# Kernel optimization log

Hardware: AMD Instinct MI355X
Metric: run time of the kernel (lower is better)

## Reference

```python
import jax, jax.numpy as jnp
import numpy as np

B, IN_E, IN_I, D = 4096, 4096, 4096, 2048
IN_BR = 8192
BS = IN_BR // D  # block size = 4
K_E, K_I = 50, 1
E_TO_I = 50.0
BN_EPS = 1e-5


def setup_inputs() -> dict:
    key = jax.random.key(0)
    ks = jax.random.split(key, 8)
    # fan-in uniform init like nn.Linear (kaiming-uniform bound ~ 1/sqrt(in))
    def linw(k, out_f, in_f):
        b = 1.0 / np.sqrt(in_f)
        return jax.random.uniform(k, (out_f, in_f), jnp.float32, -b, b)
    return {
        "excitatory_input": jax.random.normal(ks[0], (B, IN_E), jnp.float32),
        "inhibitory_input": jax.random.normal(ks[1], (B, IN_I), jnp.float32),
        "dendrite_branch_outputs": jax.random.uniform(ks[2], (B, IN_BR), jnp.float32),
        "w_exc": linw(ks[3], D, IN_E),
        "w_inh": linw(ks[4], D, IN_I),
        "w_block": linw(ks[5], D, IN_BR),
        "bn_gamma": jnp.ones((D,), jnp.float32),
        "bn_beta": jnp.zeros((D,), jnp.float32),
    }


def _topk_linear(x, w, k):
    # keep the k largest weights per output row, zero the rest, then matmul
    idx = jax.lax.top_k(w, k)[1]                          # [D, k]
    mask = jnp.zeros_like(w).at[jnp.arange(w.shape[0])[:, None], idx].set(1.0)
    return x @ (w * mask).T                               # [B, D]


def _block_linear(x, w):
    # block-diagonal mask: row c uses columns [c*BS, (c+1)*BS)
    out_f = w.shape[0]
    wb = w.reshape(out_f, out_f, BS)[jnp.arange(out_f), jnp.arange(out_f)]  # [D, BS]
    xb = x.reshape(x.shape[0], out_f, BS)                                   # [B, D, BS]
    return jnp.einsum('bds,ds->bd', xb, wb)


def reference(excitatory_input, inhibitory_input, dendrite_branch_outputs,
              w_exc, w_inh, w_block, bn_gamma, bn_beta):
    dendrite_excitation = _topk_linear(excitatory_input, w_exc, K_E)
    dendrite_inhibition = _topk_linear(inhibitory_input, w_inh, K_I)
    dendrite_depolarization = _block_linear(dendrite_branch_outputs, w_block)
    total_excitatory = dendrite_excitation + dendrite_depolarization
    # neuron_type == 'excitatory'
    act = total_excitatory - E_TO_I * dendrite_inhibition
    # BatchNorm1d, training mode: batch stats, biased variance
    mean = jnp.mean(act, axis=0)
    var = jnp.var(act, axis=0)
    act = (act - mean) * jax.lax.rsqrt(var + BN_EPS) * bn_gamma + bn_beta
    return jax.nn.sigmoid(act)
```

## Files before the change

kernel.cpp:

```cpp
#include <hip/hip_runtime.h>
#include <hip/hip_fp16.h>

#define B_     4096
#define INE_   4096
#define INBR_  8192
#define D_     2048
#define KE_    50
#define KPAD_  52
#define CAP_   512

__device__ __forceinline__ unsigned packh2(float a, float b) {
  __half2 h = __floats2half2_rn(a, b);
  return __builtin_bit_cast(unsigned, h);
}
__device__ __forceinline__ float2 unpackh2(unsigned u) {
  __half2 h = __builtin_bit_cast(__half2, u);
  return __half22float2(h);
}

__device__ void topk_body(const float* __restrict__ W, int row, int k, int kpad,
                          float hi, float t0, float vscale,
                          unsigned* __restrict__ out_off, float* __restrict__ out_val)
{
  const int t = threadIdx.x;
  const float* wr = W + (size_t)row * INE_;

  __shared__ float cval[CAP_];
  __shared__ int   ccol[CAP_];
  __shared__ int   scnt;
  __shared__ int   red[4];

  float thr = t0;
  int M = 0;
  for (int attempt = 0; attempt < 8; ++attempt) {
    int local = 0;
    #pragma unroll
    for (int j = 0; j < 4; ++j) {
      float4 w4 = *reinterpret_cast<const float4*>(wr + 4 * (t + 256 * j));
      local += (w4.x > thr) + (w4.y > thr) + (w4.z > thr) + (w4.w > thr);
    }
    #pragma unroll
    for (int off = 32; off > 0; off >>= 1) local += __shfl_down(local, off);
    if ((t & 63) == 0) red[t >> 6] = local;
    __syncthreads();
    M = red[0] + red[1] + red[2] + red[3];
    __syncthreads();
    if (M >= k && M <= CAP_) break;
    if (M < k) thr = hi - (hi - thr) * 4.0f;
    else       thr = hi - (hi - thr) * 0.5f;
  }

  if (t == 0) scnt = 0;
  __syncthreads();
  #pragma unroll
  for (int j = 0; j < 4; ++j) {
    int cbase = 4 * (t + 256 * j);
    float4 w4 = *reinterpret_cast<const float4*>(wr + cbase);
    float wv[4] = {w4.x, w4.y, w4.z, w4.w};
    #pragma unroll
    for (int q = 0; q < 4; ++q) {
      if (wv[q] > thr) {
        int pp = atomicAdd(&scnt, 1);
        if (pp < CAP_) { cval[pp] = wv[q]; ccol[pp] = cbase + q; }
      }
    }
  }
  __syncthreads();
  M = scnt < CAP_ ? scnt : CAP_;

  for (int i = t; i < M; i += 256) {
    float wi = cval[i]; int ci = ccol[i];
    int rank = 0;
    for (int m = 0; m < M; ++m) {
      float wm = cval[m]; int cm = ccol[m];
      rank += (wm > wi || (wm == wi && cm < ci)) ? 1 : 0;
    }
    if (rank < k) {
      unsigned c = (unsigned)ci;
      unsigned off = ((c >> 2) << 4) | ((c & 3u) << 14);
      float    val = wi * vscale;
      if (kpad == 1) {
        out_off[row] = off;
        out_val[row] = val;
      } else {
        size_t idx = ((size_t)(rank >> 2) * D_ + row) * 4 + (rank & 3);
        out_off[idx] = off;
        out_val[idx] = val;
      }
    }
  }
  if (kpad > 1 && t < kpad - k) {
    int slot = k + t;
    size_t idx = ((size_t)(slot >> 2) * D_ + row) * 4 + (slot & 3);
    out_off[idx] = 0u;
    out_val[idx] = 0.0f;
  }
}

__global__ __launch_bounds__(256) void prep_kernel(
    const float* __restrict__ wexc, const float* __restrict__ winh,
    const float* __restrict__ wblk,
    unsigned* __restrict__ soT, float* __restrict__ veT,
    unsigned* __restrict__ so_inh, float* __restrict__ vi_inh,
    float* __restrict__ wdiag)
{
  const int bid = blockIdx.x;
  const float hi = 0.015625f;
  if (bid < 2048) {
    topk_body(wexc, bid, KE_, KPAD_, hi, hi * (1.0f - 200.0f / 4096.0f), 1.0f,
              soT, veT);
  } else if (bid < 4096) {
    topk_body(winh, bid - 2048, 1, 1, hi, hi * (1.0f - 48.0f / 4096.0f), -50.0f,
              so_inh, vi_inh);
  } else {
    const int t = threadIdx.x;
    #pragma unroll
    for (int j = 0; j < 8; ++j) {
      int d = t + 256 * j;
      float4 w = *reinterpret_cast<const float4*>(wblk + (size_t)d * (INBR_ + 4));
      reinterpret_cast<float4*>(wdiag)[d] = w;
    }
  }
}

__device__ __forceinline__ void stage_rows8(const float* __restrict__ src,
                                            unsigned* xs, int b0, int p, int Q) {
  const float* r0p = src + (size_t)(b0 + 2 * p)     * INE_;
  const float* r1p = src + (size_t)(b0 + 2 * p + 1) * INE_;
  #pragma unroll
  for (int m = 0; m < 8; ++m) {
    int c0 = 4 * Q + 512 * m;
    float4 fa = *reinterpret_cast<const float4*>(r0p + c0);
    float4 fb = *reinterpret_cast<const float4*>(r1p + c0);
    int wb = 4 * (Q + 128 * m) + p;
    xs[wb]          = packh2(fa.x, fb.x);
    xs[wb + 4096]   = packh2(fa.y, fb.y);
    xs[wb + 8192]   = packh2(fa.z, fb.z);
    xs[wb + 12288]  = packh2(fa.w, fb.w);
  }
}

__device__ __forceinline__ uint4 ld16(const char* ldsb, unsigned off) {
  return *reinterpret_cast<const uint4*>(ldsb + off);
}

#define FMA8(R, G, WV) do {                                                \
    float2 f0 = unpackh2((G).x), f1 = unpackh2((G).y);                     \
    float2 f2 = unpackh2((G).z), f3 = unpackh2((G).w);                     \
    acc[R][0] = fmaf(f0.x, (WV), acc[R][0]);                               \
    acc[R][1] = fmaf(f0.y, (WV), acc[R][1]);                               \
    acc[R][2] = fmaf(f1.x, (WV), acc[R][2]);                               \
    acc[R][3] = fmaf(f1.y, (WV), acc[R][3]);                               \
    acc[R][4] = fmaf(f2.x, (WV), acc[R][4]);                               \
    acc[R][5] = fmaf(f2.y, (WV), acc[R][5]);                               \
    acc[R][6] = fmaf(f3.x, (WV), acc[R][6]);                               \
    acc[R][7] = fmaf(f3.y, (WV), acc[R][7]);                               \
  } while (0)

__global__ __launch_bounds__(512, 4) void ei_kernel(
    const float* __restrict__ xe, const float* __restrict__ xi,
    const unsigned* __restrict__ soT, const float* __restrict__ veT,
    const unsigned* __restrict__ so_inh, const float* __restrict__ vi_inh,
    float* __restrict__ act)
{
  __shared__ unsigned xs[16384];
  const int t  = threadIdx.x;
  const int b0 = blockIdx.x * 8;
  const int p  = t & 3;
  const int Q  = t >> 2;

  float acc[4][8];
  #pragma unroll
  for (int r = 0; r < 4; ++r)
    #pragma unroll
    for (int b = 0; b < 8; ++b) acc[r][b] = 0.0f;

  const char* ldsb = reinterpret_cast<const char*>(xs);
  const uint4*  soT4 = reinterpret_cast<const uint4*>(soT);
  const float4* veT4 = reinterpret_cast<const float4*>(veT);

  stage_rows8(xe, xs, b0, p, Q);
  __syncthreads();
  for (int ii = 0; ii < KPAD_ / 4; ++ii) {
    uint4 o[4]; float4 v[4];
    #pragma unroll
    for (int r = 0; r < 4; ++r) {
      o[r] = soT4[ii * D_ + t + 512 * r];
      v[r] = veT4[ii * D_ + t + 512 * r];
    }
    {
      uint4 g[2][4];
      #pragma unroll
      for (int rr = 0; rr < 2; ++rr) {
        g[rr][0] = ld16(ldsb, o[rr].x);
        g[rr][1] = ld16(ldsb, o[rr].y);
        g[rr][2] = ld16(ldsb, o[rr].z);
        g[rr][3] = ld16(ldsb, o[rr].w);
      }
      #pragma unroll
      for (int rr = 0; rr < 2; ++rr) {
        FMA8(rr, g[rr][0], v[rr].x);
        FMA8(rr, g[rr][1], v[rr].y);
        FMA8(rr, g[rr][2], v[rr].z);
        FMA8(rr, g[rr][3], v[rr].w);
      }
    }
    {
      uint4 g[2][4];
      #pragma unroll
      for (int rr = 0; rr < 2; ++rr) {
        g[rr][0] = ld16(ldsb, o[2 + rr].x);
        g[rr][1] = ld16(ldsb, o[2 + rr].y);
        g[rr][2] = ld16(ldsb, o[2 + rr].z);
        g[rr][3] = ld16(ldsb, o[2 + rr].w);
      }
      #pragma unroll
      for (int rr = 0; rr < 2; ++rr) {
        FMA8(2 + rr, g[rr][0], v[2 + rr].x);
        FMA8(2 + rr, g[rr][1], v[2 + rr].y);
        FMA8(2 + rr, g[rr][2], v[2 + rr].z);
        FMA8(2 + rr, g[rr][3], v[2 + rr].w);
      }
    }
  }
  __syncthreads();

  stage_rows8(xi, xs, b0, p, Q);
  unsigned oi[4]; float viv[4];
  #pragma unroll
  for (int r = 0; r < 4; ++r) {
    oi[r]  = so_inh[t + 512 * r];
    viv[r] = vi_inh[t + 512 * r];
  }
  __syncthreads();
  {
    uint4 gi[4];
    #pragma unroll
    for (int r = 0; r < 4; ++r) gi[r] = ld16(ldsb, oi[r]);
    #pragma unroll
    for (int r = 0; r < 4; ++r) FMA8(r, gi[r], viv[r]);
  }

  #pragma unroll
  for (int r = 0; r < 4; ++r) {
    const int d = t + 512 * r;
    #pragma unroll
    for (int b = 0; b < 8; ++b)
      act[(size_t)(b0 + b) * D_ + d] = acc[r][b];
  }
}

__global__ __launch_bounds__(256) void br_kernel(
    const float* __restrict__ xbr, const float* __restrict__ wdiag,
    float* __restrict__ act)
{
  const float4* xbr4 = reinterpret_cast<const float4*>(xbr);
  const float4* wd4  = reinterpret_cast<const float4*>(wdiag);
  float4*       act4 = reinterpret_cast<float4*>(act);
  const int total = B_ * D_ / 4;
  for (int i = blockIdx.x * 256 + threadIdx.x; i < total;
       i += gridDim.x * 256) {
    int b  = i >> 9;
    int dq = i & 511;
    float4 a = act4[i];
    const float4* xp = xbr4 + (size_t)b * (INBR_ / 4) + 4 * dq;
    float4 x0 = xp[0], x1 = xp[1], x2 = xp[2], x3 = xp[3];
    float4 w0 = wd4[4 * dq], w1 = wd4[4 * dq + 1],
           w2 = wd4[4 * dq + 2], w3 = wd4[4 * dq + 3];
    a.x += x0.x * w0.x + x0.y * w0.y + x0.z * w0.z + x0.w * w0.w;
    a.y += x1.x * w1.x + x1.y * w1.y + x1.z * w1.z + x1.w * w1.w;
    a.z += x2.x * w2.x + x2.y * w2.y + x2.z * w2.z + x2.w * w2.w;
    a.w += x3.x * w3.x + x3.y * w3.y + x3.z * w3.z + x3.w * w3.w;
    act4[i] = a;
  }
}

__global__ __launch_bounds__(256) void reduce_stats(
    const float* __restrict__ act, float* __restrict__ sums,
    float* __restrict__ sumsq)
{
  const int dg = blockIdx.x & 63;
  const int rg = blockIdx.x >> 6;
  const int tx = threadIdx.x & 31;
  const int ty = threadIdx.x >> 5;
  const int d  = dg * 32 + tx;

  float s = 0.0f, s2 = 0.0f;
  #pragma unroll 4
  for (int i = 0; i < 64; ++i) {
    int row = rg * 512 + ty + 8 * i;
    float a = act[(size_t)row * D_ + d];
    s += a;
    s2 = fmaf(a, a, s2);
  }
  __shared__ float ls[2][8][32];
  ls[0][ty][tx] = s;
  ls[1][ty][tx] = s2;
  __syncthreads();
  if (ty == 0) {
    #pragma unroll
    for (int j = 1; j < 8; ++j) { s += ls[0][j][tx]; s2 += ls[1][j][tx]; }
    atomicAdd(&sums[d], s);
    atomicAdd(&sumsq[d], s2);
  }
}

__global__ __launch_bounds__(256) void tail_kernel(
    float* __restrict__ act, const float* __restrict__ sums,
    const float* __restrict__ sumsq, const float* __restrict__ gamma,
    const float* __restrict__ beta)
{
  __shared__ float scsh[2 * D_];
  const int tid = threadIdx.x;
  #pragma unroll
  for (int j = 0; j < 8; ++j) {
    int d = tid + 256 * j;
    float mean = sums[d]  * (1.0f / B_);
    float var  = sumsq[d] * (1.0f / B_) - mean * mean;
    float rstd = rsqrtf(var + 1e-5f);
    float sc   = gamma[d] * rstd;
    scsh[2 * d]     = sc;
    scsh[2 * d + 1] = fmaf(-mean, sc, beta[d]);
  }
  __syncthreads();

  const int r0 = blockIdx.x * 8;
  for (int rr = 0; rr < 8; ++rr) {
    float4* rowp = reinterpret_cast<float4*>(act + (size_t)(r0 + rr) * D_);
    #pragma unroll
    for (int i2 = 0; i2 < 2; ++i2) {
      int i = tid + 256 * i2;
      float4 a = rowp[i];
      const float4* sp = reinterpret_cast<const float4*>(scsh + 8 * i);
      float4 s0 = sp[0];
      float4 s1 = sp[1];
      float z0 = fmaf(a.x, s0.x, s0.y);
      float z1 = fmaf(a.y, s0.z, s0.w);
      float z2 = fmaf(a.z, s1.x, s1.y);
      float z3 = fmaf(a.w, s1.z, s1.w);
      a.x = 1.0f / (1.0f + __expf(-z0));
      a.y = 1.0f / (1.0f + __expf(-z1));
      a.z = 1.0f / (1.0f + __expf(-z2));
      a.w = 1.0f / (1.0f + __expf(-z3));
      rowp[i] = a;
    }
  }
}

extern "C" void kernel_launch(void* const* d_in, const int* in_sizes, int n_in,
                              void* d_out, int out_size, void* d_ws, size_t ws_size,
                              hipStream_t stream) {
  const float* xe    = (const float*)d_in[0];
  const float* xi    = (const float*)d_in[1];
  const float* xbr   = (const float*)d_in[2];
  const float* wexc  = (const float*)d_in[3];
  const float* winh  = (const float*)d_in[4];
  const float* wblk  = (const float*)d_in[5];
  const float* gamma = (const float*)d_in[6];
  const float* beta  = (const float*)d_in[7];
  float* act = (float*)d_out;

  char* ws = (char*)d_ws;
  unsigned* soT    = (unsigned*)(ws + 0);
  float*    veT    = (float*)   (ws + 425984);
  unsigned* so_inh = (unsigned*)(ws + 851968);
  float*    vi_inh = (float*)   (ws + 860160);
  float*    wdiag  = (float*)   (ws + 868352);
  float*    sums   = (float*)   (ws + 901120);
  float*    sumsq  = (float*)   (ws + 909312);

  hipMemsetAsync(sums, 0, 2 * D_ * sizeof(float), stream);

  prep_kernel<<<dim3(4097), dim3(256), 0, stream>>>(
      wexc, winh, wblk, soT, veT, so_inh, vi_inh, wdiag);
  ei_kernel<<<dim3(B_ / 8), dim3(512), 0, stream>>>(
      xe, xi, soT, veT, so_inh, vi_inh, act);
  br_kernel<<<dim3(2048), dim3(256), 0, stream>>>(xbr, wdiag, act);
  reduce_stats<<<dim3(512), dim3(256), 0, stream>>>(act, sums, sumsq);
  tail_kernel<<<dim3(512), dim3(256), 0, stream>>>(
      act, sums, sumsq, gamma, beta);
}
```

Measured before the change: 135.7 us.

## Fuse branch term into EI kernel, pack top-k metadata into fp16 records

Result: faster. 131.7 us (-2.9%).

```diff
diff --git a/kernel.cpp b/kernel.cpp
--- a/kernel.cpp
+++ b/kernel.cpp
@@ -20,6 +20,7 @@
 
 __device__ void topk_body(const float* __restrict__ W, int row, int k, int kpad,
                           float hi, float t0, float vscale,
+                          uint4* __restrict__ muT,
                           unsigned* __restrict__ out_off, float* __restrict__ out_val)
 {
   const int t = threadIdx.x;
@@ -78,29 +79,29 @@
     if (rank < k) {
       unsigned c = (unsigned)ci;
       unsigned off = ((c >> 2) << 4) | ((c & 3u) << 14);
-      float    val = wi * vscale;
       if (kpad == 1) {
         out_off[row] = off;
-        out_val[row] = val;
+        out_val[row] = wi * vscale;
       } else {
-        size_t idx = ((size_t)(rank >> 2) * D_ + row) * 4 + (rank & 3);
-        out_off[idx] = off;
-        out_val[idx] = val;
+        char* rec = (char*)muT + ((size_t)(rank >> 2) * D_ + row) * 16;
+        reinterpret_cast<unsigned short*>(rec)[rank & 3] = (unsigned short)off;
+        reinterpret_cast<__half*>(rec)[4 + (rank & 3)] =
+            __float2half_rn(wi * vscale);
       }
     }
   }
   if (kpad > 1 && t < kpad - k) {
     int slot = k + t;
-    size_t idx = ((size_t)(slot >> 2) * D_ + row) * 4 + (slot & 3);
-    out_off[idx] = 0u;
-    out_val[idx] = 0.0f;
+    char* rec = (char*)muT + ((size_t)(slot >> 2) * D_ + row) * 16;
+    reinterpret_cast<unsigned short*>(rec)[slot & 3] = 0;
+    reinterpret_cast<__half*>(rec)[4 + (slot & 3)] = __float2half_rn(0.0f);
   }
 }
 
 __global__ __launch_bounds__(256) void prep_kernel(
     const float* __restrict__ wexc, const float* __restrict__ winh,
     const float* __restrict__ wblk,
-    unsigned* __restrict__ soT, float* __restrict__ veT,
+    uint4* __restrict__ muT,
     unsigned* __restrict__ so_inh, float* __restrict__ vi_inh,
     float* __restrict__ wdiag)
 {
@@ -108,10 +109,10 @@
   const float hi = 0.015625f;
   if (bid < 2048) {
     topk_body(wexc, bid, KE_, KPAD_, hi, hi * (1.0f - 200.0f / 4096.0f), 1.0f,
-              soT, veT);
+              muT, nullptr, nullptr);
   } else if (bid < 4096) {
     topk_body(winh, bid - 2048, 1, 1, hi, hi * (1.0f - 48.0f / 4096.0f), -50.0f,
-              so_inh, vi_inh);
+              nullptr, so_inh, vi_inh);
   } else {
     const int t = threadIdx.x;
     #pragma unroll
@@ -157,9 +158,10 @@
     acc[R][7] = fmaf(f3.y, (WV), acc[R][7]);                               \
   } while (0)
 
-__global__ __launch_bounds__(512, 4) void ei_kernel(
+__global__ __launch_bounds__(512, 4) void fused_ei(
     const float* __restrict__ xe, const float* __restrict__ xi,
-    const unsigned* __restrict__ soT, const float* __restrict__ veT,
+    const float* __restrict__ xbr, const float* __restrict__ wdiag,
+    const uint4* __restrict__ muT,
     const unsigned* __restrict__ so_inh, const float* __restrict__ vi_inh,
     float* __restrict__ act)
 {
@@ -176,63 +178,97 @@
     for (int b = 0; b < 8; ++b) acc[r][b] = 0.0f;
 
   const char* ldsb = reinterpret_cast<const char*>(xs);
-  const uint4*  soT4 = reinterpret_cast<const uint4*>(soT);
-  const float4* veT4 = reinterpret_cast<const float4*>(veT);
 
   stage_rows8(xe, xs, b0, p, Q);
-  __syncthreads();
+
+  float4 xia[4], xib[4];
+  {
+    const float* xr0 = xi + (size_t)(b0 + 2 * p)     * INE_;
+    const float* xr1 = xi + (size_t)(b0 + 2 * p + 1) * INE_;
+    #pragma unroll
+    for (int m = 0; m < 4; ++m) {
+      xia[m] = *reinterpret_cast<const float4*>(xr0 + 4 * Q + 512 * m);
+      xib[m] = *reinterpret_cast<const float4*>(xr1 + 4 * Q + 512 * m);
+    }
+  }
+  unsigned oi[4]; float viv[4];
+  #pragma unroll
+  for (int r = 0; r < 4; ++r) {
+    oi[r]  = so_inh[t + 512 * r];
+    viv[r] = vi_inh[t + 512 * r];
+  }
+  __syncthreads();
+
   for (int ii = 0; ii < KPAD_ / 4; ++ii) {
-    uint4 o[4]; float4 v[4];
-    #pragma unroll
-    for (int r = 0; r < 4; ++r) {
-      o[r] = soT4[ii * D_ + t + 512 * r];
-      v[r] = veT4[ii * D_ + t + 512 * r];
-    }
+    uint4 m[4];
+    #pragma unroll
+    for (int r = 0; r < 4; ++r) m[r] = muT[ii * D_ + t + 512 * r];
     {
       uint4 g[2][4];
       #pragma unroll
       for (int rr = 0; rr < 2; ++rr) {
-        g[rr][0] = ld16(ldsb, o[rr].x);
-        g[rr][1] = ld16(ldsb, o[rr].y);
-        g[rr][2] = ld16(ldsb, o[rr].z);
-        g[rr][3] = ld16(ldsb, o[rr].w);
+        g[rr][0] = ld16(ldsb, m[rr].x & 0xFFFFu);
+        g[rr][1] = ld16(ldsb, m[rr].x >> 16);
+        g[rr][2] = ld16(ldsb, m[rr].y & 0xFFFFu);
+        g[rr][3] = ld16(ldsb, m[rr].y >> 16);
       }
       #pragma unroll
       for (int rr = 0; rr < 2; ++rr) {
-        FMA8(rr, g[rr][0], v[rr].x);
-        FMA8(rr, g[rr][1], v[rr].y);
-        FMA8(rr, g[rr][2], v[rr].z);
-        FMA8(rr, g[rr][3], v[rr].w);
+        float2 vA = unpackh2(m[rr].z);
+        float2 vB = unpackh2(m[rr].w);
+        FMA8(rr, g[rr][0], vA.x);
+        FMA8(rr, g[rr][1], vA.y);
+        FMA8(rr, g[rr][2], vB.x);
+        FMA8(rr, g[rr][3], vB.y);
       }
     }
     {
       uint4 g[2][4];
       #pragma unroll
       for (int rr = 0; rr < 2; ++rr) {
-        g[rr][0] = ld16(ldsb, o[2 + rr].x);
-        g[rr][1] = ld16(ldsb, o[2 + rr].y);
-        g[rr][2] = ld16(ldsb, o[2 + rr].z);
-        g[rr][3] = ld16(ldsb, o[2 + rr].w);
+        g[rr][0] = ld16(ldsb, m[2 + rr].x & 0xFFFFu);
+        g[rr][1] = ld16(ldsb, m[2 + rr].x >> 16);
+        g[rr][2] = ld16(ldsb, m[2 + rr].y & 0xFFFFu);
+        g[rr][3] = ld16(ldsb, m[2 + rr].y >> 16);
       }
       #pragma unroll
       for (int rr = 0; rr < 2; ++rr) {
-        FMA8(2 + rr, g[rr][0], v[2 + rr].x);
-        FMA8(2 + rr, g[rr][1], v[2 + rr].y);
-        FMA8(2 + rr, g[rr][2], v[2 + rr].z);
-        FMA8(2 + rr, g[rr][3], v[2 + rr].w);
-      }
-    }
-  }
-  __syncthreads();
-
-  stage_rows8(xi, xs, b0, p, Q);
-  unsigned oi[4]; float viv[4];
-  #pragma unroll
-  for (int r = 0; r < 4; ++r) {
-    oi[r]  = so_inh[t + 512 * r];
-    viv[r] = vi_inh[t + 512 * r];
-  }
-  __syncthreads();
+        float2 vA = unpackh2(m[2 + rr].z);
+        float2 vB = unpackh2(m[2 + rr].w);
+        FMA8(2 + rr, g[rr][0], vA.x);
+        FMA8(2 + rr, g[rr][1], vA.y);
+        FMA8(2 + rr, g[rr][2], vB.x);
+        FMA8(2 + rr, g[rr][3], vB.y);
+      }
+    }
+  }
+  __syncthreads();
+
+  #pragma unroll
+  for (int m = 0; m < 4; ++m) {
+    int wb = 4 * (Q + 128 * m) + p;
+    xs[wb]          = packh2(xia[m].x, xib[m].x);
+    xs[wb + 4096]   = packh2(xia[m].y, xib[m].y);
+    xs[wb + 8192]   = packh2(xia[m].z, xib[m].z);
+    xs[wb + 12288]  = packh2(xia[m].w, xib[m].w);
+  }
+  {
+    const float* xr0 = xi + (size_t)(b0 + 2 * p)     * INE_;
+    const float* xr1 = xi + (size_t)(b0 + 2 * p + 1) * INE_;
+    #pragma unroll
+    for (int m = 4; m < 8; ++m) {
+      int c0 = 4 * Q + 512 * m;
+      float4 fa = *reinterpret_cast<const float4*>(xr0 + c0);
+      float4 fb = *reinterpret_cast<const float4*>(xr1 + c0);
+      int wb = 4 * (Q + 128 * m) + p;
+      xs[wb]          = packh2(fa.x, fb.x);
+      xs[wb + 4096]   = packh2(fa.y, fb.y);
+      xs[wb + 8192]   = packh2(fa.z, fb.z);
+      xs[wb + 12288]  = packh2(fa.w, fb.w);
+    }
+  }
+  __syncthreads();
+
   {
     uint4 gi[4];
     #pragma unroll
@@ -244,34 +280,21 @@
   #pragma unroll
   for (int r = 0; r < 4; ++r) {
     const int d = t + 512 * r;
+    float4 wb4 = reinterpret_cast<const float4*>(wdiag)[d];
+    #pragma unroll
+    for (int b = 0; b < 8; ++b) {
+      float4 xb4 = *reinterpret_cast<const float4*>(
+          xbr + (size_t)(b0 + b) * INBR_ + 4 * d);
+      acc[r][b] += xb4.x * wb4.x + xb4.y * wb4.y + xb4.z * wb4.z + xb4.w * wb4.w;
+    }
+  }
+
+  #pragma unroll
+  for (int r = 0; r < 4; ++r) {
+    const int d = t + 512 * r;
     #pragma unroll
     for (int b = 0; b < 8; ++b)
       act[(size_t)(b0 + b) * D_ + d] = acc[r][b];
-  }
-}
-
-__global__ __launch_bounds__(256) void br_kernel(
-    const float* __restrict__ xbr, const float* __restrict__ wdiag,
-    float* __restrict__ act)
-{
-  const float4* xbr4 = reinterpret_cast<const float4*>(xbr);
-  const float4* wd4  = reinterpret_cast<const float4*>(wdiag);
-  float4*       act4 = reinterpret_cast<float4*>(act);
-  const int total = B_ * D_ / 4;
-  for (int i = blockIdx.x * 256 + threadIdx.x; i < total;
-       i += gridDim.x * 256) {
-    int b  = i >> 9;
-    int dq = i & 511;
-    float4 a = act4[i];
-    const float4* xp = xbr4 + (size_t)b * (INBR_ / 4) + 4 * dq;
-    float4 x0 = xp[0], x1 = xp[1], x2 = xp[2], x3 = xp[3];
-    float4 w0 = wd4[4 * dq], w1 = wd4[4 * dq + 1],
-           w2 = wd4[4 * dq + 2], w3 = wd4[4 * dq + 3];
-    a.x += x0.x * w0.x + x0.y * w0.y + x0.z * w0.z + x0.w * w0.w;
-    a.y += x1.x * w1.x + x1.y * w1.y + x1.z * w1.z + x1.w * w1.w;
-    a.z += x2.x * w2.x + x2.y * w2.y + x2.z * w2.z + x2.w * w2.w;
-    a.w += x3.x * w3.x + x3.y * w3.y + x3.z * w3.z + x3.w * w3.w;
-    act4[i] = a;
   }
 }
 
@@ -306,9 +329,9 @@
 }
 
 __global__ __launch_bounds__(256) void tail_kernel(
-    float* __restrict__ act, const float* __restrict__ sums,
-    const float* __restrict__ sumsq, const float* __restrict__ gamma,
-    const float* __restrict__ beta)
+    const float* __restrict__ act, float* __restrict__ out,
+    const float* __restrict__ sums, const float* __restrict__ sumsq,
+    const float* __restrict__ gamma, const float* __restrict__ beta)
 {
   __shared__ float scsh[2 * D_];
   const int tid = threadIdx.x;
@@ -326,11 +349,12 @@
 
   const int r0 = blockIdx.x * 8;
   for (int rr = 0; rr < 8; ++rr) {
-    float4* rowp = reinterpret_cast<float4*>(act + (size_t)(r0 + rr) * D_);
+    const float4* ap = reinterpret_cast<const float4*>(act + (size_t)(r0 + rr) * D_);
+    float4*       op = reinterpret_cast<float4*>(out + (size_t)(r0 + rr) * D_);
     #pragma unroll
     for (int i2 = 0; i2 < 2; ++i2) {
       int i = tid + 256 * i2;
-      float4 a = rowp[i];
+      float4 a = ap[i];
       const float4* sp = reinterpret_cast<const float4*>(scsh + 8 * i);
       float4 s0 = sp[0];
       float4 s1 = sp[1];
@@ -338,11 +362,12 @@
       float z1 = fmaf(a.y, s0.z, s0.w);
       float z2 = fmaf(a.z, s1.x, s1.y);
       float z3 = fmaf(a.w, s1.z, s1.w);
-      a.x = 1.0f / (1.0f + __expf(-z0));
-      a.y = 1.0f / (1.0f + __expf(-z1));
-      a.z = 1.0f / (1.0f + __expf(-z2));
-      a.w = 1.0f / (1.0f + __expf(-z3));
-      rowp[i] = a;
+      float4 o;
+      o.x = 1.0f / (1.0f + __expf(-z0));
+      o.y = 1.0f / (1.0f + __expf(-z1));
+      o.z = 1.0f / (1.0f + __expf(-z2));
+      o.w = 1.0f / (1.0f + __expf(-z3));
+      op[i] = o;
     }
   }
 }
@@ -358,25 +383,24 @@
   const float* wblk  = (const float*)d_in[5];
   const float* gamma = (const float*)d_in[6];
   const float* beta  = (const float*)d_in[7];
-  float* act = (float*)d_out;
+  float* out = (float*)d_out;
 
   char* ws = (char*)d_ws;
-  unsigned* soT    = (unsigned*)(ws + 0);
-  float*    veT    = (float*)   (ws + 425984);
-  unsigned* so_inh = (unsigned*)(ws + 851968);
-  float*    vi_inh = (float*)   (ws + 860160);
-  float*    wdiag  = (float*)   (ws + 868352);
-  float*    sums   = (float*)   (ws + 901120);
-  float*    sumsq  = (float*)   (ws + 909312);
+  uint4*    muT    = (uint4*)   (ws + 0);
+  unsigned* so_inh = (unsigned*)(ws + 425984);
+  float*    vi_inh = (float*)   (ws + 434176);
+  float*    wdiag  = (float*)   (ws + 442368);
+  float*    sums   = (float*)   (ws + 475136);
+  float*    sumsq  = (float*)   (ws + 483328);
+  float*    act    = (float*)   (ws + 1048576);
 
   hipMemsetAsync(sums, 0, 2 * D_ * sizeof(float), stream);
 
   prep_kernel<<<dim3(4097), dim3(256), 0, stream>>>(
-      wexc, winh, wblk, soT, veT, so_inh, vi_inh, wdiag);
-  ei_kernel<<<dim3(B_ / 8), dim3(512), 0, stream>>>(
-      xe, xi, soT, veT, so_inh, vi_inh, act);
-  br_kernel<<<dim3(2048), dim3(256), 0, stream>>>(xbr, wdiag, act);
+      wexc, winh, wblk, muT, so_inh, vi_inh, wdiag);
+  fused_ei<<<dim3(B_ / 8), dim3(512), 0, stream>>>(
+      xe, xi, xbr, wdiag, muT, so_inh, vi_inh, act);
   reduce_stats<<<dim3(512), dim3(256), 0, stream>>>(act, sums, sumsq);
   tail_kernel<<<dim3(512), dim3(256), 0, stream>>>(
-      act, sums, sumsq, gamma, beta);
-}
+      act, out, sums, sumsq, gamma, beta);
+}
```
